# Kernel tuning notes

Hardware: AMD Instinct MI355X
Metric: run time of the kernel (lower is better)

Reference implementation:

```python
import jax, jax.numpy as jnp
import numpy as np

N_NODES = 100000
N_EDGES = 3200000
D_IN = 128
UNITS = 128


def setup_inputs() -> dict:
    key = jax.random.key(0)
    k1, k2, k3, k4, k5, k6 = jax.random.split(key, 6)
    x = jax.random.normal(k1, (N_NODES, D_IN), dtype=jnp.float32)
    edge_src = jax.random.randint(k2, (N_EDGES,), 0, N_NODES, dtype=jnp.int32)
    edge_dst = jax.random.randint(k3, (N_EDGES,), 0, N_NODES, dtype=jnp.int32)
    edge_vals = jax.random.uniform(k4, (N_EDGES,), dtype=jnp.float32)
    w = jax.random.normal(k5, (D_IN, UNITS), dtype=jnp.float32) * (2.0 / D_IN) ** 0.5  # he_normal scale
    b = jax.random.normal(k6, (UNITS,), dtype=jnp.float32) * 0.05
    return {"x": x, "edge_src": edge_src, "edge_dst": edge_dst,
            "edge_vals": edge_vals, "w": w, "b": b}


def reference(x, edge_src, edge_dst, edge_vals, w, b):
    # dense transform: [N, D_IN] @ [D_IN, UNITS] -> [N, UNITS]
    h = x @ w
    # sparse adjacency SpMM via edge list: out[dst] += val * h[src]
    msgs = edge_vals[:, None] * h[edge_src]  # [E, UNITS]
    agg = jax.ops.segment_sum(msgs, edge_dst, num_segments=N_NODES)
    # fused bias + relu epilogue
    return jax.nn.relu(agg + b)
```

## Files before the change

kernel.cpp:

```cpp
#include <hip/hip_runtime.h>

#define NODES 100000
#define EDGES 3200000
#define D 128
#define NBUCKET ((NODES + 255) / 256)
#define NBUCKP 392
#define CH 4096
#define NB_BIN ((EDGES + CH - 1) / CH)
#define CAP 10240

typedef unsigned short us8 __attribute__((ext_vector_type(8)));
typedef _Float16 half8 __attribute__((ext_vector_type(8)));
typedef _Float16 h2 __attribute__((ext_vector_type(2)));
typedef float f32x4 __attribute__((ext_vector_type(4)));

__device__ __forceinline__ unsigned short f32_to_f16_bits(float f) {
    return __builtin_bit_cast(unsigned short, (_Float16)f);
}
__device__ __forceinline__ h2 uh2(unsigned u) {
    return __builtin_bit_cast(h2, u);
}

__global__ __launch_bounds__(256) void wprep(const float* __restrict__ w,
                                             unsigned short* __restrict__ wt) {
    int i = blockIdx.x * 256 + threadIdx.x;
    if (i >= 16384) return;
    int j  = i & 7;
    int l  = (i >> 3) & 63;
    int c  = (i >> 9) & 3;
    int ct = i >> 11;
    int k   = 32 * c + ((l >> 4) << 3) + j;
    int col = (ct << 4) + (l & 15);
    wt[i] = f32_to_f16_bits(w[k * D + col]);
}

__global__ __launch_bounds__(256) void gemm_mfma(const float* __restrict__ x,
                                                 const unsigned short* __restrict__ wt,
                                                 unsigned short* __restrict__ hb) {
    __shared__ unsigned short wl[16384];
    const int tid = threadIdx.x;
    for (int i = tid; i < 2048; i += 256)
        ((us8*)wl)[i] = ((const us8*)wt)[i];
    __syncthreads();

    const int wave = tid >> 6, lane = tid & 63;
    const long r0 = ((long)blockIdx.x * 4 + wave) * 16;
    if (r0 >= NODES) return;
    const int m = lane & 15, q = lane >> 4;
    const float* xr = x + (r0 + m) * D;

    f32x4 acc[8];
#pragma unroll
    for (int ct = 0; ct < 8; ct++) acc[ct] = (f32x4){0.f, 0.f, 0.f, 0.f};

#pragma unroll
    for (int c = 0; c < 4; c++) {
        const int k0 = 32 * c + 8 * q;
        float4 xa = *(const float4*)(xr + k0);
        float4 xb = *(const float4*)(xr + k0 + 4);
        half8 a;
        a[0] = (_Float16)xa.x;
        a[1] = (_Float16)xa.y;
        a[2] = (_Float16)xa.z;
        a[3] = (_Float16)xa.w;
        a[4] = (_Float16)xb.x;
        a[5] = (_Float16)xb.y;
        a[6] = (_Float16)xb.z;
        a[7] = (_Float16)xb.w;
#pragma unroll
        for (int ct = 0; ct < 8; ct++) {
            half8 bfr = *(const half8*)&wl[(((ct << 2) + c) * 64 + lane) * 8];
            acc[ct] = __builtin_amdgcn_mfma_f32_16x16x32_f16(a, bfr, acc[ct], 0, 0, 0);
        }
    }

#pragma unroll
    for (int ct = 0; ct < 8; ct++) {
#pragma unroll
        for (int r = 0; r < 4; r++) {
            int row = q * 4 + r;
            hb[(r0 + row) * D + ct * 16 + m] = f32_to_f16_bits(acc[ct][r]);
        }
    }
}

__global__ __launch_bounds__(256) void init_bcur(int* __restrict__ bcur) {
    int i = blockIdx.x * 256 + threadIdx.x;
    if (i < NBUCKET) bcur[i] = i * CAP;
}

__global__ __launch_bounds__(256) void bin_pass1(const int* __restrict__ esrc,
                                                 const int* __restrict__ edst,
                                                 const float* __restrict__ eval,
                                                 int* __restrict__ bcur,
                                                 int2* __restrict__ tmp) {
    __shared__ int2 sed[CH];
    __shared__ int hist[NBUCKP];
    __shared__ int basel[NBUCKP];
    __shared__ int lcur[NBUCKP];
    __shared__ int gbase[NBUCKP];
    __shared__ int wsum[4];
    const int tid = threadIdx.x;
    const long e0 = (long)blockIdx.x * CH;
    const int n = (int)((EDGES - e0 < CH) ? (EDGES - e0) : CH);

    for (int bk = tid; bk < NBUCKP; bk += 256) { hist[bk] = 0; lcur[bk] = 0; }
    __syncthreads();
    for (int i = tid; i < n; i += 256)
        atomicAdd(&hist[edst[e0 + i] >> 8], 1);
    __syncthreads();

    int h0 = 0, h1 = 0;
    if (tid < 196) { h0 = hist[2 * tid]; h1 = hist[2 * tid + 1]; }
    int s = h0 + h1;
    int lane = tid & 63, wid = tid >> 6;
    int sc = s;
#pragma unroll
    for (int off = 1; off < 64; off <<= 1) {
        int t = __shfl_up(sc, off, 64);
        if (lane >= off) sc += t;
    }
    if (lane == 63) wsum[wid] = sc;
    __syncthreads();
    int wb = 0;
    for (int w2 = 0; w2 < wid; w2++) wb += wsum[w2];
    int excl = wb + sc - s;
    if (tid < 196) { basel[2 * tid] = excl; basel[2 * tid + 1] = excl + h0; }
    for (int bk = tid; bk < NBUCKET; bk += 256) {
        int c = hist[bk];
        if (c > 0) gbase[bk] = atomicAdd(&bcur[bk], c);
    }
    __syncthreads();

    for (int i = tid; i < n; i += 256) {
        long e = e0 + i;
        int dst = edst[e];
        unsigned hv = (unsigned)f32_to_f16_bits(eval[e]);
        unsigned pk = (hv << 17) | (unsigned)esrc[e];
        int bk = dst >> 8;
        int lp = basel[bk] + atomicAdd(&lcur[bk], 1);
        sed[lp] = make_int2((int)pk, dst);
    }
    __syncthreads();

    for (int i = tid; i < n; i += 256) {
        int2 t = sed[i];
        int bk = t.y >> 8;
        tmp[gbase[bk] + (i - basel[bk])] = t;
    }
}

__global__ __launch_bounds__(256) void bin_pass2(const int* __restrict__ bcur,
                                                 const int2* __restrict__ tmp,
                                                 int* __restrict__ rpd,
                                                 unsigned* __restrict__ epk) {
    __shared__ unsigned spk[CAP];
    __shared__ unsigned char sd8[CAP];
    __shared__ int cnt[256];
    __shared__ int pos[256];
    __shared__ int wsum[4];
    const int b = blockIdx.x;
    const int tid = threadIdx.x;
    const int beg = b * CAP;
    const int n = bcur[b] - beg;

    cnt[tid] = 0;
    __syncthreads();
    for (int i = tid; i < n; i += 256) {
        int2 t = tmp[beg + i];
        spk[i] = (unsigned)t.x;
        int d8 = t.y & 255;
        sd8[i] = (unsigned char)d8;
        atomicAdd(&cnt[d8], 1);
    }
    __syncthreads();

    int v = cnt[tid];
    int lane = tid & 63, wid = tid >> 6;
    int s = v;
#pragma unroll
    for (int off = 1; off < 64; off <<= 1) {
        int t = __shfl_up(s, off, 64);
        if (lane >= off) s += t;
    }
    if (lane == 63) wsum[wid] = s;
    __syncthreads();
    int wbase = 0;
    for (int w = 0; w < wid; w++) wbase += wsum[w];
    int excl = wbase + s - v;
    pos[tid] = excl;
    int node = (b << 8) + tid;
    if (node < NODES) rpd[node] = (((beg << 1) + excl) << 8) | v;
    __syncthreads();

    for (int i = tid; i < n; i += 256) {
        int p = atomicAdd(&pos[sd8[i]], 1);
        epk[(beg << 1) + p] = spk[i];
    }
}

__global__ __launch_bounds__(256) void aggregate(const int* __restrict__ rpd,
                                                 const unsigned* __restrict__ epack,
                                                 const unsigned short* __restrict__ hb,
                                                 const float* __restrict__ bias,
                                                 float* __restrict__ out) {
    const int lane = threadIdx.x & 63;
    const int node = blockIdx.x * 4 + (threadIdx.x >> 6);
    if (node >= NODES) return;
    const int sub = lane >> 4;
    const int li  = lane & 15;
    const int v = rpd[node];
    const int beg = (int)(((unsigned)v) >> 8);
    const int end = beg + (v & 255);
    const unsigned short* hp = hb + li * 8;

    h2 aA0 = (h2)0, aA1 = (h2)0, aA2 = (h2)0, aA3 = (h2)0;
    h2 aB0 = (h2)0, aB1 = (h2)0, aB2 = (h2)0, aB3 = (h2)0;

    for (int e0 = beg + sub; e0 < end; e0 += 16) {
        int i0 = e0, i1 = e0 + 4, i2 = e0 + 8, i3 = e0 + 12;
        unsigned p0 = epack[i0];
        unsigned p1 = (i1 < end) ? epack[i1] : 0u;
        unsigned p2 = (i2 < end) ? epack[i2] : 0u;
        unsigned p3 = (i3 < end) ? epack[i3] : 0u;

        unsigned s0 = p0 & 0x1FFFFu, s1 = p1 & 0x1FFFFu;
        unsigned s2 = p2 & 0x1FFFFu, s3 = p3 & 0x1FFFFu;
        unsigned v0 = p0 >> 17, v1 = p1 >> 17, v2 = p2 >> 17, v3 = p3 >> 17;

        uint4 r0 = *(const uint4*)(hp + (size_t)s0 * D);
        uint4 r1 = *(const uint4*)(hp + (size_t)s1 * D);
        uint4 r2 = *(const uint4*)(hp + (size_t)s2 * D);
        uint4 r3 = *(const uint4*)(hp + (size_t)s3 * D);

        h2 w0 = uh2(v0 | (v0 << 16));
        h2 w1 = uh2(v1 | (v1 << 16));
        h2 w2 = uh2(v2 | (v2 << 16));
        h2 w3 = uh2(v3 | (v3 << 16));

        aA0 = uh2(r0.x) * w0 + aA0;
        aA1 = uh2(r0.y) * w0 + aA1;
        aA2 = uh2(r0.z) * w0 + aA2;
        aA3 = uh2(r0.w) * w0 + aA3;
        aB0 = uh2(r1.x) * w1 + aB0;
        aB1 = uh2(r1.y) * w1 + aB1;
        aB2 = uh2(r1.z) * w1 + aB2;
        aB3 = uh2(r1.w) * w1 + aB3;
        aA0 = uh2(r2.x) * w2 + aA0;
        aA1 = uh2(r2.y) * w2 + aA1;
        aA2 = uh2(r2.z) * w2 + aA2;
        aA3 = uh2(r2.w) * w2 + aA3;
        aB0 = uh2(r3.x) * w3 + aB0;
        aB1 = uh2(r3.y) * w3 + aB1;
        aB2 = uh2(r3.z) * w3 + aB2;
        aB3 = uh2(r3.w) * w3 + aB3;
    }

    h2 m0 = aA0 + aB0, m1 = aA1 + aB1, m2 = aA2 + aB2, m3 = aA3 + aB3;
    float r[8];
    r[0] = (float)m0[0]; r[1] = (float)m0[1];
    r[2] = (float)m1[0]; r[3] = (float)m1[1];
    r[4] = (float)m2[0]; r[5] = (float)m2[1];
    r[6] = (float)m3[0]; r[7] = (float)m3[1];
#pragma unroll
    for (int k = 0; k < 8; k++) {
        r[k] += __shfl_xor(r[k], 16, 64);
        r[k] += __shfl_xor(r[k], 32, 64);
    }

    if (sub == 0) {
        const float* bp = bias + li * 8;
        float4 b0 = *(const float4*)bp;
        float4 b1 = *(const float4*)(bp + 4);
        float4 o0, o1;
        o0.x = fmaxf(r[0] + b0.x, 0.f);
        o0.y = fmaxf(r[1] + b0.y, 0.f);
        o0.z = fmaxf(r[2] + b0.z, 0.f);
        o0.w = fmaxf(r[3] + b0.w, 0.f);
        o1.x = fmaxf(r[4] + b1.x, 0.f);
        o1.y = fmaxf(r[5] + b1.y, 0.f);
        o1.z = fmaxf(r[6] + b1.z, 0.f);
        o1.w = fmaxf(r[7] + b1.w, 0.f);
        float* op = out + (size_t)node * D + li * 8;
        *(float4*)op = o0;
        *(float4*)(op + 4) = o1;
    }
}

extern "C" void kernel_launch(void* const* d_in, const int* in_sizes, int n_in,
                              void* d_out, int out_size, void* d_ws, size_t ws_size,
                              hipStream_t stream) {
    const float* x    = (const float*)d_in[0];
    const int*   esrc = (const int*)  d_in[1];
    const int*   edst = (const int*)  d_in[2];
    const float* eval = (const float*)d_in[3];
    const float* w    = (const float*)d_in[4];
    const float* b    = (const float*)d_in[5];
    float* out = (float*)d_out;

    char* ws = (char*)d_ws;
    const size_t OFF_H    = 0;
    const size_t OFF_WT   = 25600000;
    const size_t OFF_RPD  = OFF_WT   + 32768;
    const size_t OFF_BCUR = OFF_RPD  + 400128;
    const size_t OFF_TMP  = OFF_BCUR + 2048;

    unsigned short* hb   = (unsigned short*)(ws + OFF_H);
    unsigned short* wt   = (unsigned short*)(ws + OFF_WT);
    int*            rpd  = (int*)           (ws + OFF_RPD);
    int*            bcur = (int*)           (ws + OFF_BCUR);
    int2*           tmp  = (int2*)          (ws + OFF_TMP);
    unsigned*       epk  = (unsigned*)      (ws + OFF_TMP);

    wprep<<<64, 256, 0, stream>>>(w, wt);
    gemm_mfma<<<(NODES + 63) / 64, 256, 0, stream>>>(x, wt, hb);
    init_bcur<<<2, 256, 0, stream>>>(bcur);
    bin_pass1<<<NB_BIN, 256, 0, stream>>>(esrc, edst, eval, bcur, tmp);
    bin_pass2<<<NBUCKET, 256, 0, stream>>>(bcur, tmp, rpd, epk);
    aggregate<<<(NODES + 3) / 4, 256, 0, stream>>>(rpd, epk, hb, b, out);
}
```

Measured before the change: 307.0 us.

## Fuse GEMM and edge binning into one heterogeneous launch, drop weight-prep kernel

Merges the dense MFMA GEMM and the first edge-binning pass into a single kernel, with blocks split by blockIdx so the independent stages run concurrently. Each GEMM block now converts and swizzles the fp32 weights into LDS itself, which removes the separate wprep kernel. The bucket-cursor init kernel is replaced by a memset, and bucket cursors become relative offsets. This removes several launches and lets the compute-bound GEMM overlap the memory-bound binning. In exchange, every GEMM block redundantly re-reads and converts the 64KB weight matrix, and the shared LDS size is set by the larger of the two roles.

```diff
diff --git a/kernel.cpp b/kernel.cpp
--- a/kernel.cpp
+++ b/kernel.cpp
@@ -7,6 +7,7 @@
 #define NBUCKP 392
 #define CH 4096
 #define NB_BIN ((EDGES + CH - 1) / CH)
+#define GEMM_NB ((NODES + 63) / 64)
 #define CAP 10240
 
 typedef unsigned short us8 __attribute__((ext_vector_type(8)));
@@ -21,132 +22,123 @@
     return __builtin_bit_cast(h2, u);
 }
 
-__global__ __launch_bounds__(256) void wprep(const float* __restrict__ w,
-                                             unsigned short* __restrict__ wt) {
-    int i = blockIdx.x * 256 + threadIdx.x;
-    if (i >= 16384) return;
-    int j  = i & 7;
-    int l  = (i >> 3) & 63;
-    int c  = (i >> 9) & 3;
-    int ct = i >> 11;
-    int k   = 32 * c + ((l >> 4) << 3) + j;
-    int col = (ct << 4) + (l & 15);
-    wt[i] = f32_to_f16_bits(w[k * D + col]);
-}
-
-__global__ __launch_bounds__(256) void gemm_mfma(const float* __restrict__ x,
-                                                 const unsigned short* __restrict__ wt,
-                                                 unsigned short* __restrict__ hb) {
-    __shared__ unsigned short wl[16384];
+__global__ __launch_bounds__(256) void fusedA(const float* __restrict__ x,
+                                              const float* __restrict__ w,
+                                              const int* __restrict__ esrc,
+                                              const int* __restrict__ edst,
+                                              const float* __restrict__ eval,
+                                              int* __restrict__ bcur,
+                                              int2* __restrict__ tmp,
+                                              unsigned short* __restrict__ hb) {
+    __shared__ __align__(16) char smem[39072];
     const int tid = threadIdx.x;
-    for (int i = tid; i < 2048; i += 256)
-        ((us8*)wl)[i] = ((const us8*)wt)[i];
-    __syncthreads();
-
-    const int wave = tid >> 6, lane = tid & 63;
-    const long r0 = ((long)blockIdx.x * 4 + wave) * 16;
-    if (r0 >= NODES) return;
-    const int m = lane & 15, q = lane >> 4;
-    const float* xr = x + (r0 + m) * D;
-
-    f32x4 acc[8];
-#pragma unroll
-    for (int ct = 0; ct < 8; ct++) acc[ct] = (f32x4){0.f, 0.f, 0.f, 0.f};
-
-#pragma unroll
-    for (int c = 0; c < 4; c++) {
-        const int k0 = 32 * c + 8 * q;
-        float4 xa = *(const float4*)(xr + k0);
-        float4 xb = *(const float4*)(xr + k0 + 4);
-        half8 a;
-        a[0] = (_Float16)xa.x;
-        a[1] = (_Float16)xa.y;
-        a[2] = (_Float16)xa.z;
-        a[3] = (_Float16)xa.w;
-        a[4] = (_Float16)xb.x;
-        a[5] = (_Float16)xb.y;
-        a[6] = (_Float16)xb.z;
-        a[7] = (_Float16)xb.w;
+
+    if (blockIdx.x < NB_BIN) {
+        int2* sed   = (int2*)smem;
+        int*  hist  = (int*)(smem + 32768);
+        int*  basel = (int*)(smem + 34336);
+        int*  lcur  = (int*)(smem + 35904);
+        int*  gbase = (int*)(smem + 37472);
+        int*  wsum  = (int*)(smem + 39040);
+        const long e0 = (long)blockIdx.x * CH;
+        const int n = (int)((EDGES - e0 < CH) ? (EDGES - e0) : CH);
+
+        for (int bk = tid; bk < NBUCKP; bk += 256) { hist[bk] = 0; lcur[bk] = 0; }
+        __syncthreads();
+        for (int i = tid; i < n; i += 256)
+            atomicAdd(&hist[edst[e0 + i] >> 8], 1);
+        __syncthreads();
+
+        int h0 = 0, h1 = 0;
+        if (tid < 196) { h0 = hist[2 * tid]; h1 = hist[2 * tid + 1]; }
+        int s = h0 + h1;
+        int lane = tid & 63, wid = tid >> 6;
+        int sc = s;
+#pragma unroll
+        for (int off = 1; off < 64; off <<= 1) {
+            int t = __shfl_up(sc, off, 64);
+            if (lane >= off) sc += t;
+        }
+        if (lane == 63) wsum[wid] = sc;
+        __syncthreads();
+        int wb = 0;
+        for (int w2 = 0; w2 < wid; w2++) wb += wsum[w2];
+        int excl = wb + sc - s;
+        if (tid < 196) { basel[2 * tid] = excl; basel[2 * tid + 1] = excl + h0; }
+        for (int bk = tid; bk < NBUCKET; bk += 256) {
+            int c = hist[bk];
+            if (c > 0) gbase[bk] = bk * CAP + atomicAdd(&bcur[bk], c);
+        }
+        __syncthreads();
+
+        for (int i = tid; i < n; i += 256) {
+            long e = e0 + i;
+            int dst = edst[e];
+            unsigned hv = (unsigned)f32_to_f16_bits(eval[e]);
+            unsigned pk = (hv << 17) | (unsigned)esrc[e];
+            int bk = dst >> 8;
+            int lp = basel[bk] + atomicAdd(&lcur[bk], 1);
+            sed[lp] = make_int2((int)pk, dst);
+        }
+        __syncthreads();
+
+        for (int i = tid; i < n; i += 256) {
+            int2 t = sed[i];
+            int bk = t.y >> 8;
+            tmp[gbase[bk] + (i - basel[bk])] = t;
+        }
+    } else {
+        unsigned short* wl = (unsigned short*)smem;
+        for (int i = tid; i < 16384; i += 256) {
+            int j  = i & 7;
+            int l  = (i >> 3) & 63;
+            int c  = (i >> 9) & 3;
+            int ct = i >> 11;
+            int k   = 32 * c + ((l >> 4) << 3) + j;
+            int col = (ct << 4) + (l & 15);
+            wl[i] = f32_to_f16_bits(w[k * D + col]);
+        }
+        __syncthreads();
+
+        const int wave = tid >> 6, lane = tid & 63;
+        const long r0 = ((long)(blockIdx.x - NB_BIN) * 4 + wave) * 16;
+        if (r0 >= NODES) return;
+        const int m = lane & 15, q = lane >> 4;
+        const float* xr = x + (r0 + m) * D;
+
+        f32x4 acc[8];
+#pragma unroll
+        for (int ct = 0; ct < 8; ct++) acc[ct] = (f32x4){0.f, 0.f, 0.f, 0.f};
+
+#pragma unroll
+        for (int c = 0; c < 4; c++) {
+            const int k0 = 32 * c + 8 * q;
+            float4 xa = *(const float4*)(xr + k0);
+            float4 xb = *(const float4*)(xr + k0 + 4);
+            half8 a;
+            a[0] = (_Float16)xa.x;
+            a[1] = (_Float16)xa.y;
+            a[2] = (_Float16)xa.z;
+            a[3] = (_Float16)xa.w;
+            a[4] = (_Float16)xb.x;
+            a[5] = (_Float16)xb.y;
+            a[6] = (_Float16)xb.z;
+            a[7] = (_Float16)xb.w;
+#pragma unroll
+            for (int ct = 0; ct < 8; ct++) {
+                half8 bfr = *(const half8*)&wl[(((ct << 2) + c) * 64 + lane) * 8];
+                acc[ct] = __builtin_amdgcn_mfma_f32_16x16x32_f16(a, bfr, acc[ct], 0, 0, 0);
+            }
+        }
+
 #pragma unroll
         for (int ct = 0; ct < 8; ct++) {
-            half8 bfr = *(const half8*)&wl[(((ct << 2) + c) * 64 + lane) * 8];
-            acc[ct] = __builtin_amdgcn_mfma_f32_16x16x32_f16(a, bfr, acc[ct], 0, 0, 0);
-        }
-    }
-
-#pragma unroll
-    for (int ct = 0; ct < 8; ct++) {
-#pragma unroll
-        for (int r = 0; r < 4; r++) {
-            int row = q * 4 + r;
-            hb[(r0 + row) * D + ct * 16 + m] = f32_to_f16_bits(acc[ct][r]);
-        }
-    }
-}
-
-__global__ __launch_bounds__(256) void init_bcur(int* __restrict__ bcur) {
-    int i = blockIdx.x * 256 + threadIdx.x;
-    if (i < NBUCKET) bcur[i] = i * CAP;
-}
-
-__global__ __launch_bounds__(256) void bin_pass1(const int* __restrict__ esrc,
-                                                 const int* __restrict__ edst,
-                                                 const float* __restrict__ eval,
-                                                 int* __restrict__ bcur,
-                                                 int2* __restrict__ tmp) {
-    __shared__ int2 sed[CH];
-    __shared__ int hist[NBUCKP];
-    __shared__ int basel[NBUCKP];
-    __shared__ int lcur[NBUCKP];
-    __shared__ int gbase[NBUCKP];
-    __shared__ int wsum[4];
-    const int tid = threadIdx.x;
-    const long e0 = (long)blockIdx.x * CH;
-    const int n = (int)((EDGES - e0 < CH) ? (EDGES - e0) : CH);
-
-    for (int bk = tid; bk < NBUCKP; bk += 256) { hist[bk] = 0; lcur[bk] = 0; }
-    __syncthreads();
-    for (int i = tid; i < n; i += 256)
-        atomicAdd(&hist[edst[e0 + i] >> 8], 1);
-    __syncthreads();
-
-    int h0 = 0, h1 = 0;
-    if (tid < 196) { h0 = hist[2 * tid]; h1 = hist[2 * tid + 1]; }
-    int s = h0 + h1;
-    int lane = tid & 63, wid = tid >> 6;
-    int sc = s;
-#pragma unroll
-    for (int off = 1; off < 64; off <<= 1) {
-        int t = __shfl_up(sc, off, 64);
-        if (lane >= off) sc += t;
-    }
-    if (lane == 63) wsum[wid] = sc;
-    __syncthreads();
-    int wb = 0;
-    for (int w2 = 0; w2 < wid; w2++) wb += wsum[w2];
-    int excl = wb + sc - s;
-    if (tid < 196) { basel[2 * tid] = excl; basel[2 * tid + 1] = excl + h0; }
-    for (int bk = tid; bk < NBUCKET; bk += 256) {
-        int c = hist[bk];
-        if (c > 0) gbase[bk] = atomicAdd(&bcur[bk], c);
-    }
-    __syncthreads();
-
-    for (int i = tid; i < n; i += 256) {
-        long e = e0 + i;
-        int dst = edst[e];
-        unsigned hv = (unsigned)f32_to_f16_bits(eval[e]);
-        unsigned pk = (hv << 17) | (unsigned)esrc[e];
-        int bk = dst >> 8;
-        int lp = basel[bk] + atomicAdd(&lcur[bk], 1);
-        sed[lp] = make_int2((int)pk, dst);
-    }
-    __syncthreads();
-
-    for (int i = tid; i < n; i += 256) {
-        int2 t = sed[i];
-        int bk = t.y >> 8;
-        tmp[gbase[bk] + (i - basel[bk])] = t;
+#pragma unroll
+            for (int r = 0; r < 4; r++) {
+                int row = q * 4 + r;
+                hb[(r0 + row) * D + ct * 16 + m] = f32_to_f16_bits(acc[ct][r]);
+            }
+        }
     }
 }
 
@@ -162,7 +154,7 @@
     const int b = blockIdx.x;
     const int tid = threadIdx.x;
     const int beg = b * CAP;
-    const int n = bcur[b] - beg;
+    const int n = bcur[b];
 
     cnt[tid] = 0;
     __syncthreads();
@@ -300,22 +292,18 @@
 
     char* ws = (char*)d_ws;
     const size_t OFF_H    = 0;
-    const size_t OFF_WT   = 25600000;
-    const size_t OFF_RPD  = OFF_WT   + 32768;
+    const size_t OFF_RPD  = 25600000;
     const size_t OFF_BCUR = OFF_RPD  + 400128;
     const size_t OFF_TMP  = OFF_BCUR + 2048;
 
     unsigned short* hb   = (unsigned short*)(ws + OFF_H);
-    unsigned short* wt   = (unsigned short*)(ws + OFF_WT);
     int*            rpd  = (int*)           (ws + OFF_RPD);
     int*            bcur = (int*)           (ws + OFF_BCUR);
     int2*           tmp  = (int2*)          (ws + OFF_TMP);
     unsigned*       epk  = (unsigned*)      (ws + OFF_TMP);
 
-    wprep<<<64, 256, 0, stream>>>(w, wt);
-    gemm_mfma<<<(NODES + 63) / 64, 256, 0, stream>>>(x, wt, hb);
-    init_bcur<<<2, 256, 0, stream>>>(bcur);
-    bin_pass1<<<NB_BIN, 256, 0, stream>>>(esrc, edst, eval, bcur, tmp);
+    hipMemsetAsync(bcur, 0, NBUCKET * sizeof(int), stream);
+    fusedA<<<NB_BIN + GEMM_NB, 256, 0, stream>>>(x, w, esrc, edst, eval, bcur, tmp, hb);
     bin_pass2<<<NBUCKET, 256, 0, stream>>>(bcur, tmp, rpd, epk);
     aggregate<<<(NODES + 3) / 4, 256, 0, stream>>>(rpd, epk, hb, b, out);
 }
```

Measured after the change: 317.7 us. 3.5% more time.

## Cache edge data in registers during binning and widen bin kernels to 512 threads

Applied to the files above, without the earlier changes.

bin_pass1 now reads each edge's dst, src and value once into per-thread registers (8 per thread). It uses them for both the histogram and the local scatter, instead of re-reading dst from global memory in a second pass. Both binning kernels move to 512-thread blocks, with the scan restricted to the first 256 threads. The init_bcur kernel is replaced by a hipMemsetAsync, so bucket counters become relative offsets that are added to bk*CAP. This cuts global traffic and one launch, at the cost of higher register pressure and a barrier placed inside divergent branches in bin_pass2.

```diff
diff --git a/kernel.cpp b/kernel.cpp
--- a/kernel.cpp
+++ b/kernel.cpp
@@ -84,12 +84,7 @@
     }
 }
 
-__global__ __launch_bounds__(256) void init_bcur(int* __restrict__ bcur) {
-    int i = blockIdx.x * 256 + threadIdx.x;
-    if (i < NBUCKET) bcur[i] = i * CAP;
-}
-
-__global__ __launch_bounds__(256) void bin_pass1(const int* __restrict__ esrc,
+__global__ __launch_bounds__(512) void bin_pass1(const int* __restrict__ esrc,
                                                  const int* __restrict__ edst,
                                                  const float* __restrict__ eval,
                                                  int* __restrict__ bcur,
@@ -99,15 +94,30 @@
     __shared__ int basel[NBUCKP];
     __shared__ int lcur[NBUCKP];
     __shared__ int gbase[NBUCKP];
-    __shared__ int wsum[4];
+    __shared__ int wsum[8];
     const int tid = threadIdx.x;
     const long e0 = (long)blockIdx.x * CH;
     const int n = (int)((EDGES - e0 < CH) ? (EDGES - e0) : CH);
 
-    for (int bk = tid; bk < NBUCKP; bk += 256) { hist[bk] = 0; lcur[bk] = 0; }
-    __syncthreads();
-    for (int i = tid; i < n; i += 256)
-        atomicAdd(&hist[edst[e0 + i] >> 8], 1);
+    for (int bk = tid; bk < NBUCKP; bk += 512) { hist[bk] = 0; lcur[bk] = 0; }
+    __syncthreads();
+
+    unsigned pk[8];
+    int ds[8];
+#pragma unroll
+    for (int u = 0; u < 8; u++) {
+        int i = tid + u * 512;
+        if (i < n) {
+            long e = e0 + i;
+            int dst = edst[e];
+            unsigned hv = (unsigned)f32_to_f16_bits(eval[e]);
+            pk[u] = (hv << 17) | (unsigned)esrc[e];
+            ds[u] = dst;
+            atomicAdd(&hist[dst >> 8], 1);
+        } else {
+            ds[u] = -1;
+        }
+    }
     __syncthreads();
 
     int h0 = 0, h1 = 0;
@@ -123,34 +133,33 @@
     if (lane == 63) wsum[wid] = sc;
     __syncthreads();
     int wb = 0;
-    for (int w2 = 0; w2 < wid; w2++) wb += wsum[w2];
+    for (int w2 = 0; w2 < wid && w2 < 4; w2++) wb += wsum[w2];
     int excl = wb + sc - s;
     if (tid < 196) { basel[2 * tid] = excl; basel[2 * tid + 1] = excl + h0; }
-    for (int bk = tid; bk < NBUCKET; bk += 256) {
+    for (int bk = tid; bk < NBUCKET; bk += 512) {
         int c = hist[bk];
-        if (c > 0) gbase[bk] = atomicAdd(&bcur[bk], c);
-    }
-    __syncthreads();
-
-    for (int i = tid; i < n; i += 256) {
-        long e = e0 + i;
-        int dst = edst[e];
-        unsigned hv = (unsigned)f32_to_f16_bits(eval[e]);
-        unsigned pk = (hv << 17) | (unsigned)esrc[e];
-        int bk = dst >> 8;
-        int lp = basel[bk] + atomicAdd(&lcur[bk], 1);
-        sed[lp] = make_int2((int)pk, dst);
-    }
-    __syncthreads();
-
-    for (int i = tid; i < n; i += 256) {
+        if (c > 0) gbase[bk] = bk * CAP + atomicAdd(&bcur[bk], c);
+    }
+    __syncthreads();
+
+#pragma unroll
+    for (int u = 0; u < 8; u++) {
+        if (ds[u] >= 0) {
+            int bk = ds[u] >> 8;
+            int lp = basel[bk] + atomicAdd(&lcur[bk], 1);
+            sed[lp] = make_int2((int)pk[u], ds[u]);
+        }
+    }
+    __syncthreads();
+
+    for (int i = tid; i < n; i += 512) {
         int2 t = sed[i];
         int bk = t.y >> 8;
         tmp[gbase[bk] + (i - basel[bk])] = t;
     }
 }
 
-__global__ __launch_bounds__(256) void bin_pass2(const int* __restrict__ bcur,
+__global__ __launch_bounds__(512) void bin_pass2(const int* __restrict__ bcur,
                                                  const int2* __restrict__ tmp,
                                                  int* __restrict__ rpd,
                                                  unsigned* __restrict__ epk) {
@@ -162,11 +171,11 @@
     const int b = blockIdx.x;
     const int tid = threadIdx.x;
     const int beg = b * CAP;
-    const int n = bcur[b] - beg;
-
-    cnt[tid] = 0;
-    __syncthreads();
-    for (int i = tid; i < n; i += 256) {
+    const int n = bcur[b];
+
+    for (int i = tid; i < 256; i += 512) cnt[i] = 0;
+    __syncthreads();
+    for (int i = tid; i < n; i += 512) {
         int2 t = tmp[beg + i];
         spk[i] = (unsigned)t.x;
         int d8 = t.y & 255;
@@ -175,25 +184,29 @@
     }
     __syncthreads();
 
-    int v = cnt[tid];
-    int lane = tid & 63, wid = tid >> 6;
-    int s = v;
-#pragma unroll
-    for (int off = 1; off < 64; off <<= 1) {
-        int t = __shfl_up(s, off, 64);
-        if (lane >= off) s += t;
-    }
-    if (lane == 63) wsum[wid] = s;
-    __syncthreads();
-    int wbase = 0;
-    for (int w = 0; w < wid; w++) wbase += wsum[w];
-    int excl = wbase + s - v;
-    pos[tid] = excl;
-    int node = (b << 8) + tid;
-    if (node < NODES) rpd[node] = (((beg << 1) + excl) << 8) | v;
-    __syncthreads();
-
-    for (int i = tid; i < n; i += 256) {
+    if (tid < 256) {
+        int v = cnt[tid];
+        int lane = tid & 63, wid = tid >> 6;
+        int s = v;
+#pragma unroll
+        for (int off = 1; off < 64; off <<= 1) {
+            int t = __shfl_up(s, off, 64);
+            if (lane >= off) s += t;
+        }
+        if (lane == 63) wsum[wid] = s;
+        __syncthreads();
+        int wbase = 0;
+        for (int w = 0; w < wid; w++) wbase += wsum[w];
+        int excl = wbase + s - v;
+        pos[tid] = excl;
+        int node = (b << 8) + tid;
+        if (node < NODES) rpd[node] = (((beg << 1) + excl) << 8) | v;
+    } else {
+        __syncthreads();
+    }
+    __syncthreads();
+
+    for (int i = tid; i < n; i += 512) {
         int p = atomicAdd(&pos[sd8[i]], 1);
         epk[(beg << 1) + p] = spk[i];
     }
@@ -312,10 +325,10 @@
     int2*           tmp  = (int2*)          (ws + OFF_TMP);
     unsigned*       epk  = (unsigned*)      (ws + OFF_TMP);
 
+    hipMemsetAsync(bcur, 0, NBUCKET * sizeof(int), stream);
     wprep<<<64, 256, 0, stream>>>(w, wt);
     gemm_mfma<<<(NODES + 63) / 64, 256, 0, stream>>>(x, wt, hb);
-    init_bcur<<<2, 256, 0, stream>>>(bcur);
-    bin_pass1<<<NB_BIN, 256, 0, stream>>>(esrc, edst, eval, bcur, tmp);
-    bin_pass2<<<NBUCKET, 256, 0, stream>>>(bcur, tmp, rpd, epk);
+    bin_pass1<<<NB_BIN, 512, 0, stream>>>(esrc, edst, eval, bcur, tmp);
+    bin_pass2<<<NBUCKET, 512, 0, stream>>>(bcur, tmp, rpd, epk);
     aggregate<<<(NODES + 3) / 4, 256, 0, stream>>>(rpd, epk, hb, b, out);
 }
```

Result: faster. 293.4 us (-4.4%).
